# Kernel optimization log

Measured on AMD Instinct MI355X. Metric: run time of the kernel, lower is better.

Reference implementation:

```python
import jax, jax.numpy as jnp
import numpy as np
from jax import lax

DN = ('NHWC', 'HWIO', 'NHWC')

def _conv(x, w):
    return lax.conv_general_dilated(x, w, window_strides=(1, 1), padding='SAME', dimension_numbers=DN)

def _hard_sigmoid(z):
    # keras hard_sigmoid: clip(0.2*z + 0.5, 0, 1) -- default recurrent_activation of ConvLSTM2D
    return jnp.clip(0.2 * z + 0.5, 0.0, 1.0)

def setup_inputs() -> dict:
    key = jax.random.key(0)
    ks = jax.random.split(key, 6)
    B, T, H, W, Cin = 4, 16, 64, 64, 32
    F, kh, kw = 64, 3, 3
    x  = jax.random.normal(ks[0], (B, T, H, W, Cin), dtype=jnp.float32)
    Wx = jax.random.normal(ks[1], (kh, kw, Cin, 4 * F), dtype=jnp.float32) * 0.05
    Wh = jax.random.normal(ks[2], (kh, kw, F, 4 * F), dtype=jnp.float32) * 0.05
    b  = jnp.zeros((4 * F,), dtype=jnp.float32)
    Wp = jax.random.normal(ks[3], (1, 1, Cin, F), dtype=jnp.float32) * 0.05
    bp = jnp.zeros((F,), dtype=jnp.float32)
    return {"x": x, "Wx": Wx, "Wh": Wh, "b": b, "Wp": Wp, "bp": bp}

def reference(x, Wx, Wh, b, Wp, bp):
    B, T, H, W, Cin = x.shape
    F = Wh.shape[2]
    # Precompute the input-to-gate convolutions for all timesteps at once.
    zx = _conv(x.reshape(B * T, H, W, Cin), Wx) + b          # (B*T, H, W, 4F)
    zx = zx.reshape(B, T, H, W, 4 * F).transpose(1, 0, 2, 3, 4)  # time-major

    def step(carry, zx_t):
        h, c = carry
        z = zx_t + _conv(h, Wh)                              # (B, H, W, 4F)
        zi, zf, zc, zo = jnp.split(z, 4, axis=-1)            # keras gate order i,f,c,o
        i = _hard_sigmoid(zi)
        f = _hard_sigmoid(zf)
        c_new = f * c + i * jnp.tanh(zc)
        o = _hard_sigmoid(zo)
        h_new = o * jnp.tanh(c_new)
        return (h_new, c_new), h_new

    h0 = jnp.zeros((B, H, W, F), dtype=x.dtype)
    c0 = jnp.zeros((B, H, W, F), dtype=x.dtype)
    _, hs = lax.scan(step, (h0, c0), zx)                     # (T, B, H, W, F)
    convlstm_out = hs.transpose(1, 0, 2, 3, 4)               # (B, T, H, W, F)

    # TimeDistributed 1x1 projection of the input as the residual branch.
    residual = _conv(x.reshape(B * T, H, W, Cin), Wp) + bp
    residual = residual.reshape(B, T, H, W, F)
    return convlstm_out + residual
```

## Files before the change

### kernel.cpp

```cpp
#include <hip/hip_runtime.h>

#define B_ 4
#define T_ 16
#define H_ 64
#define W_ 64
#define CIN 32
#define F_ 64
#define NCH 256
#define KSTEPS 27
#define TSLAB (H_ * W_ * F_)

#define OFF_H0 557056
#define OFF_H1 2654208

typedef __attribute__((ext_vector_type(8))) short short8;
typedef __attribute__((ext_vector_type(4))) float floatx4;
typedef __attribute__((address_space(3))) unsigned int  lds_u32;
typedef __attribute__((address_space(1))) const unsigned int g_u32;

__device__ __forceinline__ unsigned short f2bf(float f) {
  union { float f; unsigned u; } v; v.f = f;
  unsigned r = v.u + 0x7FFFu + ((v.u >> 16) & 1u);
  return (unsigned short)(r >> 16);
}

__device__ __forceinline__ float tanh_fast(float z) {
  float e = __expf(2.0f * z);
  return 1.0f - 2.0f * __builtin_amdgcn_rcpf(e + 1.0f);
}

__global__ void prep_weights(const float* __restrict__ Wx, const float* __restrict__ Wh,
                             unsigned short* __restrict__ WT) {
  int idx = blockIdx.x * 256 + threadIdx.x;
  int s = idx / 10240;
  int r = idx - s * 10240;
  int n = r / 40;
  int c = r - n * 40;
  unsigned short v = 0;
  if (c < 32) {
    int k  = s * 32 + c;
    int g  = k / 96;
    int ch = k - g * 96;
    float f = (ch < CIN) ? Wx[(g * CIN + ch) * NCH + n]
                         : Wh[(g * F_ + (ch - CIN)) * NCH + n];
    v = f2bf(f);
  }
  WT[idx] = v;
}

__global__ void prep_zero_h(float4* __restrict__ p) {
  int idx = blockIdx.x * 256 + threadIdx.x;
  p[idx] = make_float4(0.f, 0.f, 0.f, 0.f);
}

__global__ void prep_zero_c(float* __restrict__ out) {
  int idx = blockIdx.x * 256 + threadIdx.x;
  int b = idx >> 16;
  int i = idx & 65535;
  ((float4*)(out + (size_t)b * (T_ * TSLAB)))[i] = make_float4(0.f, 0.f, 0.f, 0.f);
}

__device__ __forceinline__ void stage_wt(const unsigned short* __restrict__ src,
                                         short* dstbuf, int w, int lane) {
  __attribute__((address_space(3))) unsigned short* d =
      (__attribute__((address_space(3))) unsigned short*)dstbuf + w * 2560;
  const unsigned short* s = src + w * 2560 + lane * 8;
  #pragma unroll
  for (int q = 0; q < 5; q++)
    __builtin_amdgcn_global_load_lds((g_u32*)(s + q * 512), (lds_u32*)(d + q * 512),
                                     16, 0, 0);
}

__global__ __launch_bounds__(256, 2)
void step_kernel(const float* __restrict__ x, const float* __restrict__ bias,
                 const float* __restrict__ Wp, const float* __restrict__ bp,
                 const unsigned short* __restrict__ WT,
                 const unsigned short* __restrict__ hprev,
                 unsigned short* __restrict__ hnew,
                 float* __restrict__ out, int t)
{
  __shared__ __align__(16) char smem[62176];
  short* patch = (short*)smem;
  short* bl0   = (short*)(smem + 21216);
  short* bl1   = (short*)(smem + 41696);
  float* gact  = (float*)smem;
  float* WpL   = (float*)(smem + 49152);

  const int tid  = threadIdx.x;
  const int w    = tid >> 6;
  const int lane = tid & 63;
  const int quad = lane >> 4;
  const int lr   = lane & 15;

  const int bid = blockIdx.x;
  const int b   = bid >> 7;
  const int rem = bid & 127;
  const int y0  = rem >> 1;
  const int x0  = (rem & 1) << 5;

  stage_wt(WT, bl0, w, lane);

  if (tid < 102) {
    int sy = tid / 34, sx = tid - sy * 34;
    int yy = y0 + sy - 1, xx = x0 + sx - 1;
    short* dst = patch + tid * 104;
    if (yy >= 0 && yy < H_ && xx >= 0 && xx < W_) {
      const float4* xs = (const float4*)(x + ((((b * T_ + t) * H_ + yy) * W_ + xx) * CIN));
      #pragma unroll
      for (int j = 0; j < 4; j++) {
        float4 f0 = xs[2 * j];
        float4 f1 = xs[2 * j + 1];
        union { short8 v; unsigned short u[8]; } pk;
        pk.u[0] = f2bf(f0.x); pk.u[1] = f2bf(f0.y); pk.u[2] = f2bf(f0.z); pk.u[3] = f2bf(f0.w);
        pk.u[4] = f2bf(f1.x); pk.u[5] = f2bf(f1.y); pk.u[6] = f2bf(f1.z); pk.u[7] = f2bf(f1.w);
        ((short8*)dst)[j] = pk.v;
      }
      const uint4* hs = (const uint4*)(hprev + ((b * H_ + yy) * W_ + xx) * F_);
      uint4* d2 = (uint4*)(dst + 32);
      #pragma unroll
      for (int j = 0; j < 8; j++) d2[j] = hs[j];
    } else {
      uint4 z = make_uint4(0, 0, 0, 0);
      uint4* d4 = (uint4*)dst;
      #pragma unroll
      for (int j = 0; j < 12; j++) d4[j] = z;
    }
  }

  float bias_r[4];
  #pragma unroll
  for (int nf = 0; nf < 4; nf++) bias_r[nf] = bias[w * 64 + nf * 16 + lr];

  floatx4 acc[2][4];
  #pragma unroll
  for (int mf = 0; mf < 2; mf++)
    #pragma unroll
    for (int nf = 0; nf < 4; nf++)
      acc[mf][nf] = (floatx4){0.f, 0.f, 0.f, 0.f};

  __syncthreads();

  const unsigned short* wsrc = WT + 10240;
  for (int s = 0; s < KSTEPS; s++) {
    short* cur = (s & 1) ? bl1 : bl0;
    if (s < KSTEPS - 1) {
      stage_wt(wsrc, (s & 1) ? bl0 : bl1, w, lane);
      wsrc += 10240;
    }
    int g  = s / 3;
    int c0 = (s - g * 3) * 32;
    int dy = g / 3, dx = g - dy * 3;
    short8 afr[2], bfr[4];
    #pragma unroll
    for (int mf = 0; mf < 2; mf++) {
      int tx = mf * 16 + lr;
      afr[mf] = *(const short8*)(patch + (dy * 34 + tx + dx) * 104 + c0 + quad * 8);
    }
    #pragma unroll
    for (int nf = 0; nf < 4; nf++) {
      int n = w * 64 + nf * 16 + lr;
      bfr[nf] = *(const short8*)(cur + n * 40 + quad * 8);
    }
    #pragma unroll
    for (int mf = 0; mf < 2; mf++)
      #pragma unroll
      for (int nf = 0; nf < 4; nf++)
        acc[mf][nf] = __builtin_amdgcn_mfma_f32_16x16x32_bf16(afr[mf], bfr[nf], acc[mf][nf], 0, 0, 0);
    __syncthreads();
  }

  #pragma unroll
  for (int mf = 0; mf < 2; mf++)
    #pragma unroll
    for (int nf = 0; nf < 4; nf++)
      #pragma unroll
      for (int r = 0; r < 4; r++) {
        int p = mf * 16 + quad * 4 + r;
        float z = acc[mf][nf][r] + bias_r[nf];
        float a;
        if (w == 2) a = tanh_fast(z);
        else {
          a = __builtin_fmaf(z, 0.2f, 0.5f);
          a = fminf(fmaxf(a, 0.f), 1.f);
        }
        gact[(w * 64 + nf * 16 + lr) * 37 + p] = a;
      }
  {
    float4* d = (float4*)WpL;
    const float4* sWp = (const float4*)Wp;
    d[tid * 2]     = sWp[tid * 2];
    d[tid * 2 + 1] = sWp[tid * 2 + 1];
  }

  const int mloc = tid >> 3;
  const int cb   = (tid & 7) * 8;
  const int gy   = y0, gx = x0 + mloc;
  const int hbase   = ((b * H_ + gy) * W_ + gx) * F_ + cb;
  const int outbase = (((b * T_ + t) * H_ + gy) * W_ + gx) * F_ + cb;

  float xv[32];
  {
    const float4* xs = (const float4*)(x + ((((b * T_ + t) * H_ + gy) * W_ + gx) * CIN));
    #pragma unroll
    for (int j = 0; j < 8; j++) {
      float4 f = xs[j];
      xv[4 * j] = f.x; xv[4 * j + 1] = f.y; xv[4 * j + 2] = f.z; xv[4 * j + 3] = f.w;
    }
  }
  float4 co4[2];
  #pragma unroll
  for (int j = 0; j < 2; j++) co4[j] = *(const float4*)(out + outbase + 4 * j);

  __syncthreads();

  float res[8];
  #pragma unroll
  for (int j = 0; j < 8; j++) res[j] = bp[cb + j];
  for (int ci = 0; ci < 32; ci++) {
    float xf = xv[ci];
    #pragma unroll
    for (int j4 = 0; j4 < 2; j4++) {
      float4 wv = *(const float4*)(WpL + ci * 64 + cb + j4 * 4);
      res[j4 * 4 + 0] += xf * wv.x;
      res[j4 * 4 + 1] += xf * wv.y;
      res[j4 * 4 + 2] += xf * wv.z;
      res[j4 * 4 + 3] += xf * wv.w;
    }
  }

  float iv[8], fv[8], gv[8], ov[8];
  #pragma unroll
  for (int j = 0; j < 8; j++) {
    iv[j] = gact[(0 * 64 + cb + j) * 37 + mloc];
    fv[j] = gact[(1 * 64 + cb + j) * 37 + mloc];
    gv[j] = gact[(2 * 64 + cb + j) * 37 + mloc];
    ov[j] = gact[(3 * 64 + cb + j) * 37 + mloc];
  }
  union { unsigned short hv[8]; uint4 q; } hu;
  #pragma unroll
  for (int j4 = 0; j4 < 2; j4++) {
    float cold[4] = {j4 ? co4[1].x : co4[0].x, j4 ? co4[1].y : co4[0].y,
                     j4 ? co4[1].z : co4[0].z, j4 ? co4[1].w : co4[0].w};
    float cn4[4], h4[4];
    #pragma unroll
    for (int e = 0; e < 4; e++) {
      int j = j4 * 4 + e;
      float cn = fv[j] * cold[e] + iv[j] * gv[j];
      float h  = ov[j] * tanh_fast(cn);
      cn4[e] = cn; h4[e] = h;
      hu.hv[j] = f2bf(h);
    }
    if (t < T_ - 1)
      *(float4*)(out + outbase + TSLAB + j4 * 4) = make_float4(cn4[0], cn4[1], cn4[2], cn4[3]);
    *(float4*)(out + outbase + j4 * 4) = make_float4(h4[0] + res[j4 * 4 + 0], h4[1] + res[j4 * 4 + 1],
                                                     h4[2] + res[j4 * 4 + 2], h4[3] + res[j4 * 4 + 3]);
  }
  *(uint4*)(hnew + hbase) = hu.q;
}

extern "C" void kernel_launch(void* const* d_in, const int* in_sizes, int n_in,
                              void* d_out, int out_size, void* d_ws, size_t ws_size,
                              hipStream_t stream) {
  const float* x    = (const float*)d_in[0];
  const float* Wx   = (const float*)d_in[1];
  const float* Wh   = (const float*)d_in[2];
  const float* bias = (const float*)d_in[3];
  const float* Wp   = (const float*)d_in[4];
  const float* bp   = (const float*)d_in[5];
  float* out = (float*)d_out;

  unsigned short* WT = (unsigned short*)d_ws;
  unsigned short* h0 = (unsigned short*)((char*)d_ws + OFF_H0);
  unsigned short* h1 = (unsigned short*)((char*)d_ws + OFF_H1);

  hipLaunchKernelGGL(prep_weights, dim3(1080), dim3(256), 0, stream, Wx, Wh, WT);
  hipLaunchKernelGGL(prep_zero_h, dim3(1024), dim3(256), 0, stream,
                     (float4*)((char*)d_ws + OFF_H0));
  hipLaunchKernelGGL(prep_zero_c, dim3(1024), dim3(256), 0, stream, out);

  for (int t = 0; t < T_; t++) {
    const unsigned short* hp = (t & 1) ? h1 : h0;
    unsigned short*       hn = (t & 1) ? h0 : h1;
    hipLaunchKernelGGL(step_kernel, dim3(512), dim3(256), 0, stream,
                       x, bias, Wp, bp, WT, hp, hn, out, t);
  }
}
```

Before: 780.9 us.

## Retile step kernel to 64-pixel by 128-channel tiles with register-streamed weights

Each block now covers a 2x32 pixel tile and half of the feature channels (fb split), so the grid stays at 512 blocks. Weights are re-laid out K-contiguous per output column and streamed straight from global memory into registers with one-step prefetch, which removes the double-buffered LDS weight staging and the per-k-step __syncthreads. Shared memory drops from about 62 KB to 37 KB and launch bounds rise to 4 blocks per CU for more occupancy. The gate activation buffer is transposed so the epilogue reads it with float4 loads. The cost is more global/L2 weight traffic per block and some register pressure.

```diff
diff --git a/kernel.cpp b/kernel.cpp
--- a/kernel.cpp
+++ b/kernel.cpp
@@ -7,6 +7,7 @@
 #define CIN 32
 #define F_ 64
 #define NCH 256
+#define KTOT 864
 #define KSTEPS 27
 #define TSLAB (H_ * W_ * F_)
 
@@ -15,8 +16,6 @@
 
 typedef __attribute__((ext_vector_type(8))) short short8;
 typedef __attribute__((ext_vector_type(4))) float floatx4;
-typedef __attribute__((address_space(3))) unsigned int  lds_u32;
-typedef __attribute__((address_space(1))) const unsigned int g_u32;
 
 __device__ __forceinline__ unsigned short f2bf(float f) {
   union { float f; unsigned u; } v; v.f = f;
@@ -30,22 +29,17 @@
 }
 
 __global__ void prep_weights(const float* __restrict__ Wx, const float* __restrict__ Wh,
-                             unsigned short* __restrict__ WT) {
+                             unsigned short* __restrict__ WT2) {
   int idx = blockIdx.x * 256 + threadIdx.x;
-  int s = idx / 10240;
-  int r = idx - s * 10240;
-  int n = r / 40;
-  int c = r - n * 40;
-  unsigned short v = 0;
-  if (c < 32) {
-    int k  = s * 32 + c;
-    int g  = k / 96;
-    int ch = k - g * 96;
-    float f = (ch < CIN) ? Wx[(g * CIN + ch) * NCH + n]
-                         : Wh[(g * F_ + (ch - CIN)) * NCH + n];
-    v = f2bf(f);
-  }
-  WT[idx] = v;
+  int np = idx / KTOT;
+  int k  = idx - np * KTOT;
+  int fb = np >> 7, g = (np >> 5) & 3, fi = np & 31;
+  int n  = g * 64 + fb * 32 + fi;
+  int tap = k / 96;
+  int ch  = k - tap * 96;
+  float f = (ch < CIN) ? Wx[(tap * CIN + ch) * NCH + n]
+                       : Wh[(tap * F_ + (ch - CIN)) * NCH + n];
+  WT2[idx] = f2bf(f);
 }
 
 __global__ void prep_zero_h(float4* __restrict__ p) {
@@ -60,31 +54,18 @@
   ((float4*)(out + (size_t)b * (T_ * TSLAB)))[i] = make_float4(0.f, 0.f, 0.f, 0.f);
 }
 
-__device__ __forceinline__ void stage_wt(const unsigned short* __restrict__ src,
-                                         short* dstbuf, int w, int lane) {
-  __attribute__((address_space(3))) unsigned short* d =
-      (__attribute__((address_space(3))) unsigned short*)dstbuf + w * 2560;
-  const unsigned short* s = src + w * 2560 + lane * 8;
-  #pragma unroll
-  for (int q = 0; q < 5; q++)
-    __builtin_amdgcn_global_load_lds((g_u32*)(s + q * 512), (lds_u32*)(d + q * 512),
-                                     16, 0, 0);
-}
-
-__global__ __launch_bounds__(256, 2)
+__global__ __launch_bounds__(256, 4)
 void step_kernel(const float* __restrict__ x, const float* __restrict__ bias,
                  const float* __restrict__ Wp, const float* __restrict__ bp,
-                 const unsigned short* __restrict__ WT,
+                 const unsigned short* __restrict__ WT2,
                  const unsigned short* __restrict__ hprev,
                  unsigned short* __restrict__ hnew,
                  float* __restrict__ out, int t)
 {
-  __shared__ __align__(16) char smem[62176];
+  __shared__ __align__(16) char smem[37376];
   short* patch = (short*)smem;
-  short* bl0   = (short*)(smem + 21216);
-  short* bl1   = (short*)(smem + 41696);
   float* gact  = (float*)smem;
-  float* WpL   = (float*)(smem + 49152);
+  float* WpL   = (float*)(smem + 33280);
 
   const int tid  = threadIdx.x;
   const int w    = tid >> 6;
@@ -93,14 +74,20 @@
   const int lr   = lane & 15;
 
   const int bid = blockIdx.x;
-  const int b   = bid >> 7;
-  const int rem = bid & 127;
-  const int y0  = rem >> 1;
-  const int x0  = (rem & 1) << 5;
-
-  stage_wt(WT, bl0, w, lane);
-
-  if (tid < 102) {
+  const int fb  = bid & 1;
+  const int mt  = bid >> 1;
+  const int b   = mt >> 6;
+  const int r   = mt & 63;
+  const int y0  = (r >> 1) << 1;
+  const int x0  = (r & 1) << 5;
+
+  const unsigned short* wp0 = WT2 + (fb * 128 + w * 32 + lr) * KTOT + quad * 8;
+  const unsigned short* wp1 = wp0 + 16 * KTOT;
+
+  short8 bcur0 = *(const short8*)(wp0);
+  short8 bcur1 = *(const short8*)(wp1);
+
+  if (tid < 136) {
     int sy = tid / 34, sx = tid - sy * 34;
     int yy = y0 + sy - 1, xx = x0 + sx - 1;
     short* dst = patch + tid * 104;
@@ -127,74 +114,76 @@
     }
   }
 
-  float bias_r[4];
-  #pragma unroll
-  for (int nf = 0; nf < 4; nf++) bias_r[nf] = bias[w * 64 + nf * 16 + lr];
-
-  floatx4 acc[2][4];
-  #pragma unroll
-  for (int mf = 0; mf < 2; mf++)
-    #pragma unroll
-    for (int nf = 0; nf < 4; nf++)
+  float bias_r[2];
+  #pragma unroll
+  for (int nf = 0; nf < 2; nf++) bias_r[nf] = bias[w * 64 + fb * 32 + nf * 16 + lr];
+
+  int paoff[4];
+  #pragma unroll
+  for (int mf = 0; mf < 4; mf++) {
+    int p = mf * 16 + lr;
+    paoff[mf] = ((p >> 5) * 34 + (p & 31)) * 104 + quad * 8;
+  }
+
+  floatx4 acc[4][2];
+  #pragma unroll
+  for (int mf = 0; mf < 4; mf++)
+    #pragma unroll
+    for (int nf = 0; nf < 2; nf++)
       acc[mf][nf] = (floatx4){0.f, 0.f, 0.f, 0.f};
 
   __syncthreads();
 
-  const unsigned short* wsrc = WT + 10240;
+  #pragma unroll
   for (int s = 0; s < KSTEPS; s++) {
-    short* cur = (s & 1) ? bl1 : bl0;
+    short8 bnx0, bnx1;
     if (s < KSTEPS - 1) {
-      stage_wt(wsrc, (s & 1) ? bl0 : bl1, w, lane);
-      wsrc += 10240;
-    }
-    int g  = s / 3;
-    int c0 = (s - g * 3) * 32;
-    int dy = g / 3, dx = g - dy * 3;
-    short8 afr[2], bfr[4];
-    #pragma unroll
-    for (int mf = 0; mf < 2; mf++) {
-      int tx = mf * 16 + lr;
-      afr[mf] = *(const short8*)(patch + (dy * 34 + tx + dx) * 104 + c0 + quad * 8);
-    }
-    #pragma unroll
-    for (int nf = 0; nf < 4; nf++) {
-      int n = w * 64 + nf * 16 + lr;
-      bfr[nf] = *(const short8*)(cur + n * 40 + quad * 8);
-    }
-    #pragma unroll
-    for (int mf = 0; mf < 2; mf++)
-      #pragma unroll
-      for (int nf = 0; nf < 4; nf++)
-        acc[mf][nf] = __builtin_amdgcn_mfma_f32_16x16x32_bf16(afr[mf], bfr[nf], acc[mf][nf], 0, 0, 0);
-    __syncthreads();
-  }
-
-  #pragma unroll
-  for (int mf = 0; mf < 2; mf++)
-    #pragma unroll
-    for (int nf = 0; nf < 4; nf++)
-      #pragma unroll
-      for (int r = 0; r < 4; r++) {
-        int p = mf * 16 + quad * 4 + r;
-        float z = acc[mf][nf][r] + bias_r[nf];
+      bnx0 = *(const short8*)(wp0 + (s + 1) * 32);
+      bnx1 = *(const short8*)(wp1 + (s + 1) * 32);
+    }
+    const int g  = s / 3;
+    const int c0 = (s - g * 3) * 32;
+    const int koff = ((g / 3) * 34 + (g % 3)) * 104 + c0;
+    short8 afr[4];
+    #pragma unroll
+    for (int mf = 0; mf < 4; mf++)
+      afr[mf] = *(const short8*)(patch + paoff[mf] + koff);
+    #pragma unroll
+    for (int mf = 0; mf < 4; mf++) {
+      acc[mf][0] = __builtin_amdgcn_mfma_f32_16x16x32_bf16(afr[mf], bcur0, acc[mf][0], 0, 0, 0);
+      acc[mf][1] = __builtin_amdgcn_mfma_f32_16x16x32_bf16(afr[mf], bcur1, acc[mf][1], 0, 0, 0);
+    }
+    bcur0 = bnx0;
+    bcur1 = bnx1;
+  }
+
+  __syncthreads();
+
+  #pragma unroll
+  for (int mf = 0; mf < 4; mf++)
+    #pragma unroll
+    for (int nf = 0; nf < 2; nf++)
+      #pragma unroll
+      for (int rr = 0; rr < 4; rr++) {
+        int p = mf * 16 + quad * 4 + rr;
+        float z = acc[mf][nf][rr] + bias_r[nf];
         float a;
         if (w == 2) a = tanh_fast(z);
         else {
           a = __builtin_fmaf(z, 0.2f, 0.5f);
           a = fminf(fmaxf(a, 0.f), 1.f);
         }
-        gact[(w * 64 + nf * 16 + lr) * 37 + p] = a;
+        gact[p * 130 + w * 32 + nf * 16 + lr] = a;
       }
   {
-    float4* d = (float4*)WpL;
-    const float4* sWp = (const float4*)Wp;
-    d[tid * 2]     = sWp[tid * 2];
-    d[tid * 2 + 1] = sWp[tid * 2 + 1];
-  }
-
-  const int mloc = tid >> 3;
-  const int cb   = (tid & 7) * 8;
-  const int gy   = y0, gx = x0 + mloc;
+    ((float4*)WpL)[tid] = *(const float4*)(Wp + (tid >> 3) * 64 + fb * 32 + (tid & 7) * 4);
+  }
+
+  const int p   = tid >> 2;
+  const int fh  = tid & 3;
+  const int fl  = fh * 8;
+  const int cb  = fb * 32 + fl;
+  const int gy  = y0 + (p >> 5), gx = x0 + (p & 31);
   const int hbase   = ((b * H_ + gy) * W_ + gx) * F_ + cb;
   const int outbase = (((b * T_ + t) * H_ + gy) * W_ + gx) * F_ + cb;
 
@@ -220,7 +209,7 @@
     float xf = xv[ci];
     #pragma unroll
     for (int j4 = 0; j4 < 2; j4++) {
-      float4 wv = *(const float4*)(WpL + ci * 64 + cb + j4 * 4);
+      float4 wv = *(const float4*)(WpL + ci * 32 + fl + j4 * 4);
       res[j4 * 4 + 0] += xf * wv.x;
       res[j4 * 4 + 1] += xf * wv.y;
       res[j4 * 4 + 2] += xf * wv.z;
@@ -230,11 +219,15 @@
 
   float iv[8], fv[8], gv[8], ov[8];
   #pragma unroll
-  for (int j = 0; j < 8; j++) {
-    iv[j] = gact[(0 * 64 + cb + j) * 37 + mloc];
-    fv[j] = gact[(1 * 64 + cb + j) * 37 + mloc];
-    gv[j] = gact[(2 * 64 + cb + j) * 37 + mloc];
-    ov[j] = gact[(3 * 64 + cb + j) * 37 + mloc];
+  for (int j4 = 0; j4 < 2; j4++) {
+    float4 a0 = *(const float4*)(gact + p * 130 +  0 + fl + j4 * 4);
+    float4 a1 = *(const float4*)(gact + p * 130 + 32 + fl + j4 * 4);
+    float4 a2 = *(const float4*)(gact + p * 130 + 64 + fl + j4 * 4);
+    float4 a3 = *(const float4*)(gact + p * 130 + 96 + fl + j4 * 4);
+    iv[j4*4+0]=a0.x; iv[j4*4+1]=a0.y; iv[j4*4+2]=a0.z; iv[j4*4+3]=a0.w;
+    fv[j4*4+0]=a1.x; fv[j4*4+1]=a1.y; fv[j4*4+2]=a1.z; fv[j4*4+3]=a1.w;
+    gv[j4*4+0]=a2.x; gv[j4*4+1]=a2.y; gv[j4*4+2]=a2.z; gv[j4*4+3]=a2.w;
+    ov[j4*4+0]=a3.x; ov[j4*4+1]=a3.y; ov[j4*4+2]=a3.z; ov[j4*4+3]=a3.w;
   }
   union { unsigned short hv[8]; uint4 q; } hu;
   #pragma unroll
@@ -269,11 +262,11 @@
   const float* bp   = (const float*)d_in[5];
   float* out = (float*)d_out;
 
-  unsigned short* WT = (unsigned short*)d_ws;
-  unsigned short* h0 = (unsigned short*)((char*)d_ws + OFF_H0);
-  unsigned short* h1 = (unsigned short*)((char*)d_ws + OFF_H1);
-
-  hipLaunchKernelGGL(prep_weights, dim3(1080), dim3(256), 0, stream, Wx, Wh, WT);
+  unsigned short* WT2 = (unsigned short*)d_ws;
+  unsigned short* h0  = (unsigned short*)((char*)d_ws + OFF_H0);
+  unsigned short* h1  = (unsigned short*)((char*)d_ws + OFF_H1);
+
+  hipLaunchKernelGGL(prep_weights, dim3(864), dim3(256), 0, stream, Wx, Wh, WT2);
   hipLaunchKernelGGL(prep_zero_h, dim3(1024), dim3(256), 0, stream,
                      (float4*)((char*)d_ws + OFF_H0));
   hipLaunchKernelGGL(prep_zero_c, dim3(1024), dim3(256), 0, stream, out);
@@ -282,6 +275,6 @@
     const unsigned short* hp = (t & 1) ? h1 : h0;
     unsigned short*       hn = (t & 1) ? h0 : h1;
     hipLaunchKernelGGL(step_kernel, dim3(512), dim3(256), 0, stream,
-                       x, bias, Wp, bp, WT, hp, hn, out, t);
-  }
-}
+                       x, bias, Wp, bp, WT2, hp, hn, out, t);
+  }
+}
```

Result: slower. 1.004 ms (+28.5%).

## Fuse all timesteps into one cooperative persistent kernel with LDS-resident weights

Applied to the files above, without the earlier changes.

Replaces the sixteen per-timestep launches with a single cooperative kernel of 256 blocks. Each block keeps its quarter of the gate weights resident in LDS, holds the cell state in registers, and uses a grid barrier between timesteps. It also moves the residual 1x1 projection onto MFMA by reusing the centre-tap A fragments, and stops writing and re-reading the cell state in the output buffer. This removes repeated weight streaming, launch overhead and cell-state traffic, at the cost of about 154KB of LDS per block (one block per CU), grid-sync latency and recomputing the input patch in four blocks per tile.

```diff
diff --git a/kernel.cpp b/kernel.cpp
--- a/kernel.cpp
+++ b/kernel.cpp
@@ -1,4 +1,7 @@
 #include <hip/hip_runtime.h>
+#include <hip/hip_cooperative_groups.h>
+
+namespace cg = cooperative_groups;
 
 #define B_ 4
 #define T_ 16
@@ -8,10 +11,14 @@
 #define F_ 64
 #define NCH 256
 #define KSTEPS 27
-#define TSLAB (H_ * W_ * F_)
-
-#define OFF_H0 557056
-#define OFF_H1 2654208
+
+#define OFF_H0 458752
+#define OFF_H1 2555904
+
+#define L_WLDS  0
+#define L_WPB   111616
+#define L_PATCH 112896
+#define SMEM_BYTES 157952
 
 typedef __attribute__((ext_vector_type(8))) short short8;
 typedef __attribute__((ext_vector_type(4))) float floatx4;
@@ -30,22 +37,27 @@
 }
 
 __global__ void prep_weights(const float* __restrict__ Wx, const float* __restrict__ Wh,
-                             unsigned short* __restrict__ WT) {
+                             const float* __restrict__ Wp, unsigned short* __restrict__ img) {
   int idx = blockIdx.x * 256 + threadIdx.x;
-  int s = idx / 10240;
-  int r = idx - s * 10240;
-  int n = r / 40;
-  int c = r - n * 40;
   unsigned short v = 0;
-  if (c < 32) {
-    int k  = s * 32 + c;
-    int g  = k / 96;
-    int ch = k - g * 96;
-    float f = (ch < CIN) ? Wx[(g * CIN + ch) * NCH + n]
-                         : Wh[(g * F_ + (ch - CIN)) * NCH + n];
-    v = f2bf(f);
-  }
-  WT[idx] = v;
+  if (idx < 223232) {
+    int q = idx / 55808; int r = idx - q * 55808;
+    int nloc = r / 872;  int k = r - nloc * 872;
+    if (k < 864) {
+      int g = nloc >> 4, fi = nloc & 15;
+      int n = g * 64 + q * 16 + fi;
+      int tap = k / 96, ch = k - tap * 96;
+      float f = (ch < CIN) ? Wx[(tap * CIN + ch) * NCH + n]
+                           : Wh[(tap * F_ + (ch - CIN)) * NCH + n];
+      v = f2bf(f);
+    }
+  } else {
+    int r = idx - 223232;
+    int q = r / 640; int r2 = r - q * 640;
+    int fi = r2 / 40; int c = r2 - fi * 40;
+    if (c < 32) v = f2bf(Wp[c * F_ + q * 16 + fi]);
+  }
+  img[idx] = v;
 }
 
 __global__ void prep_zero_h(float4* __restrict__ p) {
@@ -53,38 +65,18 @@
   p[idx] = make_float4(0.f, 0.f, 0.f, 0.f);
 }
 
-__global__ void prep_zero_c(float* __restrict__ out) {
-  int idx = blockIdx.x * 256 + threadIdx.x;
-  int b = idx >> 16;
-  int i = idx & 65535;
-  ((float4*)(out + (size_t)b * (T_ * TSLAB)))[i] = make_float4(0.f, 0.f, 0.f, 0.f);
-}
-
-__device__ __forceinline__ void stage_wt(const unsigned short* __restrict__ src,
-                                         short* dstbuf, int w, int lane) {
-  __attribute__((address_space(3))) unsigned short* d =
-      (__attribute__((address_space(3))) unsigned short*)dstbuf + w * 2560;
-  const unsigned short* s = src + w * 2560 + lane * 8;
-  #pragma unroll
-  for (int q = 0; q < 5; q++)
-    __builtin_amdgcn_global_load_lds((g_u32*)(s + q * 512), (lds_u32*)(d + q * 512),
-                                     16, 0, 0);
-}
-
-__global__ __launch_bounds__(256, 2)
-void step_kernel(const float* __restrict__ x, const float* __restrict__ bias,
-                 const float* __restrict__ Wp, const float* __restrict__ bp,
-                 const unsigned short* __restrict__ WT,
-                 const unsigned short* __restrict__ hprev,
-                 unsigned short* __restrict__ hnew,
-                 float* __restrict__ out, int t)
+__global__ __launch_bounds__(256)
+void lstm_all(const float* __restrict__ x, const float* __restrict__ bias,
+              const float* __restrict__ bp, const unsigned short* __restrict__ wimg,
+              unsigned short* __restrict__ h0g, unsigned short* __restrict__ h1g,
+              float* __restrict__ out)
 {
-  __shared__ __align__(16) char smem[62176];
-  short* patch = (short*)smem;
-  short* bl0   = (short*)(smem + 21216);
-  short* bl1   = (short*)(smem + 41696);
-  float* gact  = (float*)smem;
-  float* WpL   = (float*)(smem + 49152);
+  extern __shared__ __align__(16) char smem[];
+  short* wlds  = (short*)(smem + L_WLDS);
+  short* wpb   = (short*)(smem + L_WPB);
+  short* patch = (short*)(smem + L_PATCH);
+  float* gact  = (float*)(smem + L_PATCH);
+  float* resl  = (float*)(smem + L_PATCH + 34816);
 
   const int tid  = threadIdx.x;
   const int w    = tid >> 6;
@@ -93,169 +85,173 @@
   const int lr   = lane & 15;
 
   const int bid = blockIdx.x;
-  const int b   = bid >> 7;
-  const int rem = bid & 127;
-  const int y0  = rem >> 1;
-  const int x0  = (rem & 1) << 5;
-
-  stage_wt(WT, bl0, w, lane);
-
-  if (tid < 102) {
-    int sy = tid / 34, sx = tid - sy * 34;
-    int yy = y0 + sy - 1, xx = x0 + sx - 1;
-    short* dst = patch + tid * 104;
-    if (yy >= 0 && yy < H_ && xx >= 0 && xx < W_) {
-      const float4* xs = (const float4*)(x + ((((b * T_ + t) * H_ + yy) * W_ + xx) * CIN));
-      #pragma unroll
-      for (int j = 0; j < 4; j++) {
-        float4 f0 = xs[2 * j];
-        float4 f1 = xs[2 * j + 1];
-        union { short8 v; unsigned short u[8]; } pk;
-        pk.u[0] = f2bf(f0.x); pk.u[1] = f2bf(f0.y); pk.u[2] = f2bf(f0.z); pk.u[3] = f2bf(f0.w);
-        pk.u[4] = f2bf(f1.x); pk.u[5] = f2bf(f1.y); pk.u[6] = f2bf(f1.z); pk.u[7] = f2bf(f1.w);
-        ((short8*)dst)[j] = pk.v;
-      }
-      const uint4* hs = (const uint4*)(hprev + ((b * H_ + yy) * W_ + xx) * F_);
-      uint4* d2 = (uint4*)(dst + 32);
-      #pragma unroll
-      for (int j = 0; j < 8; j++) d2[j] = hs[j];
-    } else {
-      uint4 z = make_uint4(0, 0, 0, 0);
-      uint4* d4 = (uint4*)dst;
-      #pragma unroll
-      for (int j = 0; j < 12; j++) d4[j] = z;
+  const int q   = bid & 3;
+  const int grp = bid >> 2;
+  const int b   = grp >> 4;
+  const int y0  = (grp & 15) << 2;
+
+  {
+    const unsigned short* src = wimg + q * 55808;
+    __attribute__((address_space(3))) unsigned short* d =
+        (__attribute__((address_space(3))) unsigned short*)wlds;
+    for (int j = w; j < 109; j += 4)
+      __builtin_amdgcn_global_load_lds((g_u32*)(src + j * 512 + lane * 8),
+                                       (lds_u32*)(d + j * 512 + lane * 8), 16, 0, 0);
+  }
+  if (tid < 80) {
+    uint4 v = *(const uint4*)(wimg + 223232 + q * 640 + tid * 8);
+    *(uint4*)(wpb + tid * 8) = v;
+  }
+
+  float bias_r[4];
+  #pragma unroll
+  for (int nf = 0; nf < 4; nf++) bias_r[nf] = bias[nf * 64 + q * 16 + lr];
+  const float bp_r = bp[q * 16 + lr];
+
+  int paoff[2];
+  #pragma unroll
+  for (int mf = 0; mf < 2; mf++) {
+    int p = (w * 2 + mf) * 16 + lr;
+    paoff[mf] = ((p >> 5) * 34 + (p & 31)) * 104 + quad * 8;
+  }
+  int wboff[4];
+  #pragma unroll
+  for (int nf = 0; nf < 4; nf++) wboff[nf] = (nf * 16 + lr) * 872 + quad * 8;
+  const int wpoff = lr * 40 + quad * 8;
+
+  float cst[2][8];
+  #pragma unroll
+  for (int pp = 0; pp < 2; pp++)
+    #pragma unroll
+    for (int j = 0; j < 8; j++) cst[pp][j] = 0.f;
+
+  #pragma unroll 1
+  for (int t = 0; t < T_; ++t) {
+    const unsigned short* hp = (t & 1) ? h1g : h0g;
+    unsigned short*       hn = (t & 1) ? h0g : h1g;
+
+    #pragma unroll
+    for (int pp = 0; pp < 2; ++pp) {
+      const int xbase = pp << 5;
+      __syncthreads();
+
+      if (tid < 204) {
+        int sy = tid / 34, sx = tid - sy * 34;
+        int yy = y0 + sy - 1, xx = xbase + sx - 1;
+        short* dst = patch + tid * 104;
+        if (yy >= 0 && yy < H_ && xx >= 0 && xx < W_) {
+          const float4* xs = (const float4*)(x + ((((b * T_ + t) * H_ + yy) * W_ + xx) * CIN));
+          #pragma unroll
+          for (int j = 0; j < 4; j++) {
+            float4 f0 = xs[2 * j];
+            float4 f1 = xs[2 * j + 1];
+            union { short8 v; unsigned short u[8]; } pk;
+            pk.u[0] = f2bf(f0.x); pk.u[1] = f2bf(f0.y); pk.u[2] = f2bf(f0.z); pk.u[3] = f2bf(f0.w);
+            pk.u[4] = f2bf(f1.x); pk.u[5] = f2bf(f1.y); pk.u[6] = f2bf(f1.z); pk.u[7] = f2bf(f1.w);
+            ((short8*)dst)[j] = pk.v;
+          }
+          const uint4* hs = (const uint4*)(hp + ((b * H_ + yy) * W_ + xx) * F_);
+          uint4* d2 = (uint4*)(dst + 32);
+          #pragma unroll
+          for (int j = 0; j < 8; j++) d2[j] = hs[j];
+        } else {
+          uint4 z = make_uint4(0, 0, 0, 0);
+          uint4* d4 = (uint4*)dst;
+          #pragma unroll
+          for (int j = 0; j < 12; j++) d4[j] = z;
+        }
+      }
+      __syncthreads();
+
+      floatx4 acc[2][4], accr[2];
+      #pragma unroll
+      for (int mf = 0; mf < 2; mf++) {
+        accr[mf] = (floatx4){0.f, 0.f, 0.f, 0.f};
+        #pragma unroll
+        for (int nf = 0; nf < 4; nf++) acc[mf][nf] = (floatx4){0.f, 0.f, 0.f, 0.f};
+      }
+      #pragma unroll
+      for (int s = 0; s < KSTEPS; ++s) {
+        const int g3 = s / 3;
+        const int c0 = (s - g3 * 3) * 32;
+        const int koff = ((g3 / 3) * 34 + (g3 % 3)) * 104 + c0;
+        short8 afr[2];
+        afr[0] = *(const short8*)(patch + paoff[0] + koff);
+        afr[1] = *(const short8*)(patch + paoff[1] + koff);
+        #pragma unroll
+        for (int nf = 0; nf < 4; nf++) {
+          short8 bfr = *(const short8*)(wlds + wboff[nf] + s * 32);
+          acc[0][nf] = __builtin_amdgcn_mfma_f32_16x16x32_bf16(afr[0], bfr, acc[0][nf], 0, 0, 0);
+          acc[1][nf] = __builtin_amdgcn_mfma_f32_16x16x32_bf16(afr[1], bfr, acc[1][nf], 0, 0, 0);
+        }
+        if (s == 12) {
+          short8 br = *(const short8*)(wpb + wpoff);
+          accr[0] = __builtin_amdgcn_mfma_f32_16x16x32_bf16(afr[0], br, accr[0], 0, 0, 0);
+          accr[1] = __builtin_amdgcn_mfma_f32_16x16x32_bf16(afr[1], br, accr[1], 0, 0, 0);
+        }
+      }
+      __syncthreads();
+
+      #pragma unroll
+      for (int mf = 0; mf < 2; mf++) {
+        #pragma unroll
+        for (int nf = 0; nf < 4; nf++)
+          #pragma unroll
+          for (int r = 0; r < 4; r++) {
+            int px = (w * 2 + mf) * 16 + quad * 4 + r;
+            float z = acc[mf][nf][r] + bias_r[nf];
+            float a;
+            if (nf == 2) a = tanh_fast(z);
+            else {
+              a = __builtin_fmaf(z, 0.2f, 0.5f);
+              a = fminf(fmaxf(a, 0.f), 1.f);
+            }
+            gact[px * 68 + nf * 16 + lr] = a;
+          }
+        #pragma unroll
+        for (int r = 0; r < 4; r++) {
+          int px = (w * 2 + mf) * 16 + quad * 4 + r;
+          resl[px * 20 + lr] = accr[mf][r] + bp_r;
+        }
+      }
+      __syncthreads();
+
+      const int px = tid >> 1;
+      const int fo = (tid & 1) << 3;
+      const int gy = y0 + (px >> 5), gx = xbase + (px & 31);
+      const int hbase = ((b * H_ + gy) * W_ + gx) * F_ + q * 16 + fo;
+      const int outb  = (((b * T_ + t) * H_ + gy) * W_ + gx) * F_ + q * 16 + fo;
+      union { unsigned short hv[8]; uint4 u; } hu;
+      #pragma unroll
+      for (int j4 = 0; j4 < 2; ++j4) {
+        float4 gi = *(const float4*)(gact + px * 68 +  0 + fo + j4 * 4);
+        float4 gf = *(const float4*)(gact + px * 68 + 16 + fo + j4 * 4);
+        float4 gg = *(const float4*)(gact + px * 68 + 32 + fo + j4 * 4);
+        float4 go = *(const float4*)(gact + px * 68 + 48 + fo + j4 * 4);
+        float4 rs = *(const float4*)(resl + px * 20 + fo + j4 * 4);
+        float ivv[4] = {gi.x, gi.y, gi.z, gi.w};
+        float fvv[4] = {gf.x, gf.y, gf.z, gf.w};
+        float gvv[4] = {gg.x, gg.y, gg.z, gg.w};
+        float ovv[4] = {go.x, go.y, go.z, go.w};
+        float rsv[4] = {rs.x, rs.y, rs.z, rs.w};
+        float o4[4];
+        #pragma unroll
+        for (int e = 0; e < 4; ++e) {
+          int j = j4 * 4 + e;
+          float cn = fvv[e] * cst[pp][j] + ivv[e] * gvv[e];
+          float h  = ovv[e] * tanh_fast(cn);
+          cst[pp][j] = cn;
+          hu.hv[j] = f2bf(h);
+          o4[e] = h + rsv[e];
+        }
+        *(float4*)(out + outb + j4 * 4) = make_float4(o4[0], o4[1], o4[2], o4[3]);
+      }
+      *(uint4*)(hn + hbase) = hu.u;
     }
-  }
-
-  float bias_r[4];
-  #pragma unroll
-  for (int nf = 0; nf < 4; nf++) bias_r[nf] = bias[w * 64 + nf * 16 + lr];
-
-  floatx4 acc[2][4];
-  #pragma unroll
-  for (int mf = 0; mf < 2; mf++)
-    #pragma unroll
-    for (int nf = 0; nf < 4; nf++)
-      acc[mf][nf] = (floatx4){0.f, 0.f, 0.f, 0.f};
-
-  __syncthreads();
-
-  const unsigned short* wsrc = WT + 10240;
-  for (int s = 0; s < KSTEPS; s++) {
-    short* cur = (s & 1) ? bl1 : bl0;
-    if (s < KSTEPS - 1) {
-      stage_wt(wsrc, (s & 1) ? bl0 : bl1, w, lane);
-      wsrc += 10240;
-    }
-    int g  = s / 3;
-    int c0 = (s - g * 3) * 32;
-    int dy = g / 3, dx = g - dy * 3;
-    short8 afr[2], bfr[4];
-    #pragma unroll
-    for (int mf = 0; mf < 2; mf++) {
-      int tx = mf * 16 + lr;
-      afr[mf] = *(const short8*)(patch + (dy * 34 + tx + dx) * 104 + c0 + quad * 8);
-    }
-    #pragma unroll
-    for (int nf = 0; nf < 4; nf++) {
-      int n = w * 64 + nf * 16 + lr;
-      bfr[nf] = *(const short8*)(cur + n * 40 + quad * 8);
-    }
-    #pragma unroll
-    for (int mf = 0; mf < 2; mf++)
-      #pragma unroll
-      for (int nf = 0; nf < 4; nf++)
-        acc[mf][nf] = __builtin_amdgcn_mfma_f32_16x16x32_bf16(afr[mf], bfr[nf], acc[mf][nf], 0, 0, 0);
-    __syncthreads();
-  }
-
-  #pragma unroll
-  for (int mf = 0; mf < 2; mf++)
-    #pragma unroll
-    for (int nf = 0; nf < 4; nf++)
-      #pragma unroll
-      for (int r = 0; r < 4; r++) {
-        int p = mf * 16 + quad * 4 + r;
-        float z = acc[mf][nf][r] + bias_r[nf];
-        float a;
-        if (w == 2) a = tanh_fast(z);
-        else {
-          a = __builtin_fmaf(z, 0.2f, 0.5f);
-          a = fminf(fmaxf(a, 0.f), 1.f);
-        }
-        gact[(w * 64 + nf * 16 + lr) * 37 + p] = a;
-      }
-  {
-    float4* d = (float4*)WpL;
-    const float4* sWp = (const float4*)Wp;
-    d[tid * 2]     = sWp[tid * 2];
-    d[tid * 2 + 1] = sWp[tid * 2 + 1];
-  }
-
-  const int mloc = tid >> 3;
-  const int cb   = (tid & 7) * 8;
-  const int gy   = y0, gx = x0 + mloc;
-  const int hbase   = ((b * H_ + gy) * W_ + gx) * F_ + cb;
-  const int outbase = (((b * T_ + t) * H_ + gy) * W_ + gx) * F_ + cb;
-
-  float xv[32];
-  {
-    const float4* xs = (const float4*)(x + ((((b * T_ + t) * H_ + gy) * W_ + gx) * CIN));
-    #pragma unroll
-    for (int j = 0; j < 8; j++) {
-      float4 f = xs[j];
-      xv[4 * j] = f.x; xv[4 * j + 1] = f.y; xv[4 * j + 2] = f.z; xv[4 * j + 3] = f.w;
-    }
-  }
-  float4 co4[2];
-  #pragma unroll
-  for (int j = 0; j < 2; j++) co4[j] = *(const float4*)(out + outbase + 4 * j);
-
-  __syncthreads();
-
-  float res[8];
-  #pragma unroll
-  for (int j = 0; j < 8; j++) res[j] = bp[cb + j];
-  for (int ci = 0; ci < 32; ci++) {
-    float xf = xv[ci];
-    #pragma unroll
-    for (int j4 = 0; j4 < 2; j4++) {
-      float4 wv = *(const float4*)(WpL + ci * 64 + cb + j4 * 4);
-      res[j4 * 4 + 0] += xf * wv.x;
-      res[j4 * 4 + 1] += xf * wv.y;
-      res[j4 * 4 + 2] += xf * wv.z;
-      res[j4 * 4 + 3] += xf * wv.w;
-    }
-  }
-
-  float iv[8], fv[8], gv[8], ov[8];
-  #pragma unroll
-  for (int j = 0; j < 8; j++) {
-    iv[j] = gact[(0 * 64 + cb + j) * 37 + mloc];
-    fv[j] = gact[(1 * 64 + cb + j) * 37 + mloc];
-    gv[j] = gact[(2 * 64 + cb + j) * 37 + mloc];
-    ov[j] = gact[(3 * 64 + cb + j) * 37 + mloc];
-  }
-  union { unsigned short hv[8]; uint4 q; } hu;
-  #pragma unroll
-  for (int j4 = 0; j4 < 2; j4++) {
-    float cold[4] = {j4 ? co4[1].x : co4[0].x, j4 ? co4[1].y : co4[0].y,
-                     j4 ? co4[1].z : co4[0].z, j4 ? co4[1].w : co4[0].w};
-    float cn4[4], h4[4];
-    #pragma unroll
-    for (int e = 0; e < 4; e++) {
-      int j = j4 * 4 + e;
-      float cn = fv[j] * cold[e] + iv[j] * gv[j];
-      float h  = ov[j] * tanh_fast(cn);
-      cn4[e] = cn; h4[e] = h;
-      hu.hv[j] = f2bf(h);
-    }
-    if (t < T_ - 1)
-      *(float4*)(out + outbase + TSLAB + j4 * 4) = make_float4(cn4[0], cn4[1], cn4[2], cn4[3]);
-    *(float4*)(out + outbase + j4 * 4) = make_float4(h4[0] + res[j4 * 4 + 0], h4[1] + res[j4 * 4 + 1],
-                                                     h4[2] + res[j4 * 4 + 2], h4[3] + res[j4 * 4 + 3]);
-  }
-  *(uint4*)(hnew + hbase) = hu.q;
+
+    __threadfence();
+    cg::this_grid().sync();
+  }
 }
 
 extern "C" void kernel_launch(void* const* d_in, const int* in_sizes, int n_in,
@@ -269,19 +265,22 @@
   const float* bp   = (const float*)d_in[5];
   float* out = (float*)d_out;
 
-  unsigned short* WT = (unsigned short*)d_ws;
-  unsigned short* h0 = (unsigned short*)((char*)d_ws + OFF_H0);
-  unsigned short* h1 = (unsigned short*)((char*)d_ws + OFF_H1);
-
-  hipLaunchKernelGGL(prep_weights, dim3(1080), dim3(256), 0, stream, Wx, Wh, WT);
-  hipLaunchKernelGGL(prep_zero_h, dim3(1024), dim3(256), 0, stream,
+  unsigned short* wimg = (unsigned short*)d_ws;
+  unsigned short* h0   = (unsigned short*)((char*)d_ws + OFF_H0);
+  unsigned short* h1   = (unsigned short*)((char*)d_ws + OFF_H1);
+
+  hipFuncSetAttribute(reinterpret_cast<const void*>(lstm_all),
+                      hipFuncAttributeMaxDynamicSharedMemorySize, SMEM_BYTES);
+
+  hipLaunchKernelGGL(prep_weights, dim3(882), dim3(256), 0, stream, Wx, Wh, Wp, wimg);
+  hipLaunchKernelGGL(prep_zero_h, dim3(512), dim3(256), 0, stream,
                      (float4*)((char*)d_ws + OFF_H0));
-  hipLaunchKernelGGL(prep_zero_c, dim3(1024), dim3(256), 0, stream, out);
-
-  for (int t = 0; t < T_; t++) {
-    const unsigned short* hp = (t & 1) ? h1 : h0;
-    unsigned short*       hn = (t & 1) ? h0 : h1;
-    hipLaunchKernelGGL(step_kernel, dim3(512), dim3(256), 0, stream,
-                       x, bias, Wp, bp, WT, hp, hn, out, t);
-  }
-}
+
+  const float* xa = x; const float* ba = bias; const float* bpa = bp;
+  const unsigned short* wa = wimg;
+  unsigned short* h0a = h0; unsigned short* h1a = h1;
+  float* oa = out;
+  void* args[] = {&xa, &ba, &bpa, &wa, &h0a, &h1a, &oa};
+  hipLaunchCooperativeKernel(reinterpret_cast<const void*>(lstm_all),
+                             dim3(256), dim3(256), args, SMEM_BYTES, stream);
+}
```

Result: slower. 1.402 ms (+79.5%).
